# Kernel optimization log

Hardware: AMD Instinct MI355X
Metric: run time of the kernel (lower is better)

The kernel has to match this reference:

```python
import jax, jax.numpy as jnp
import numpy as np

T, B, IN, H, OUT = 16384, 1, 32, 512, 1


def setup_inputs() -> dict:
    key = jax.random.key(0)
    ks = jax.random.split(key, 7)
    s = 0.05
    return {
        "input_seq": jax.random.normal(ks[0], (T, B, IN), dtype=jnp.float32),
        "W_ih": jax.random.normal(ks[1], (4 * H, IN), dtype=jnp.float32) * s,
        "W_hh": jax.random.normal(ks[2], (4 * H, H), dtype=jnp.float32) * s,
        "b_ih": jax.random.normal(ks[3], (4 * H,), dtype=jnp.float32) * s,
        "b_hh": jax.random.normal(ks[4], (4 * H,), dtype=jnp.float32) * s,
        "W_lin": jax.random.normal(ks[5], (OUT, H), dtype=jnp.float32) * s,
        "b_lin": jax.random.normal(ks[6], (OUT,), dtype=jnp.float32) * s,
    }


def reference(input_seq, W_ih, W_hh, b_ih, b_hh, W_lin, b_lin):
    # input_seq: [T, 1, IN]; batch=1 as hardcoded by the module's hidden_cell.
    t = input_seq.shape[0]
    x = input_seq.reshape(t, -1)  # [T, IN]
    h_dim = W_hh.shape[1]
    # Precompute input contribution to gates for all timesteps (one big GEMM).
    x_gates = x @ W_ih.T + (b_ih + b_hh)  # [T, 4H]

    def step(carry, xg):
        h, c = carry
        g = xg + W_hh @ h  # [4H]; PyTorch gate order: i, f, g, o
        i = jax.nn.sigmoid(g[:h_dim])
        f = jax.nn.sigmoid(g[h_dim:2 * h_dim])
        gg = jnp.tanh(g[2 * h_dim:3 * h_dim])
        o = jax.nn.sigmoid(g[3 * h_dim:])
        c_new = f * c + i * gg
        h_new = o * jnp.tanh(c_new)
        return (h_new, c_new), h_new

    h0 = jnp.zeros((h_dim,), dtype=input_seq.dtype)
    c0 = jnp.zeros((h_dim,), dtype=input_seq.dtype)
    _, lstm_out = jax.lax.scan(step, (h0, c0), x_gates)  # [T, H]
    predictions = lstm_out @ W_lin.T + b_lin  # [T, OUT]
    return predictions[-1]  # [OUT]
```

## Files before the change

### kernel.cpp

```cpp
#include <hip/hip_runtime.h>
#include <math.h>


#define T_STEPS 16384
#define IN_DIM  32
#define H_DIM   512
#define KWG     32
#define H_SLICE 16
#define KTOT    544
#define CHUNK   136

__device__ __forceinline__ float fast_sigmoid(float v) {
  return 1.0f / (1.0f + __expf(-v));
}
__device__ __forceinline__ float fast_tanh(float v) {
  return 2.0f / (1.0f + __expf(-2.0f * v)) - 1.0f;
}

__launch_bounds__(256, 1)
__global__ void lstm_scan_kernel(
    const float* __restrict__ x,
    const float* __restrict__ Wih,
    const float* __restrict__ Whh,
    const float* __restrict__ bih,
    const float* __restrict__ bhh,
    const float* __restrict__ Wlin,
    const float* __restrict__ blin,
    float* __restrict__ out,
    unsigned long long* pub)
{
  const int wg  = blockIdx.x;
  const int tid = threadIdx.x;
  const int w   = tid >> 6;
  const int l   = tid & 63;

  __shared__ __align__(16) float hshm[KTOT];
  __shared__ float red[256];

  const int R = (l >> 4) * H_DIM + wg * H_SLICE + (l & 15);

  float wreg[CHUNK];
  #pragma unroll
  for (int j = 0; j < CHUNK; ++j) {
    const int k = w * CHUNK + j;
    wreg[j] = (k < H_DIM) ? Whh[R * H_DIM + k]
                          : Wih[R * IN_DIM + (k - H_DIM)];
  }
  const float bias = (w == 0) ? (bih[R] + bhh[R]) : 0.0f;

  float c = 0.0f;

  const int  e0 = tid * 2, e1 = tid * 2 + 1;
  const bool own0 = (e0 >> 4) == wg, own1 = (e1 >> 4) == wg;
  if (own0) hshm[e0] = 0.0f;
  if (own1) hshm[e1] = 0.0f;

  for (int t = 0; t < T_STEPS; ++t) {
    float xv = (tid < IN_DIM) ? x[t * IN_DIM + tid] : 0.0f;

    {
      const unsigned long long* p = pub + (t & 1) * H_DIM;
      const unsigned int tg = (unsigned int)t;
      bool need0 = !own0, need1 = !own1;
      while (need0 | need1) {
        if (need0) {
          unsigned long long u = __hip_atomic_load(p + e0, __ATOMIC_RELAXED,
                                                   __HIP_MEMORY_SCOPE_AGENT);
          if ((unsigned int)(u >> 32) == tg) {
            hshm[e0] = __uint_as_float((unsigned int)u);
            need0 = false;
          }
        }
        if (need1) {
          unsigned long long u = __hip_atomic_load(p + e1, __ATOMIC_RELAXED,
                                                   __HIP_MEMORY_SCOPE_AGENT);
          if ((unsigned int)(u >> 32) == tg) {
            hshm[e1] = __uint_as_float((unsigned int)u);
            need1 = false;
          }
        }
      }
      if (tid < IN_DIM) hshm[H_DIM + tid] = xv;
    }
    __syncthreads();

    const float4* hv = (const float4*)(hshm + w * CHUNK);
    float a0 = 0.f, a1 = 0.f, a2 = 0.f, a3 = 0.f;
    #pragma unroll
    for (int q = 0; q < CHUNK / 4; ++q) {
      const float4 h4 = hv[q];
      a0 = fmaf(wreg[4 * q + 0], h4.x, a0);
      a1 = fmaf(wreg[4 * q + 1], h4.y, a1);
      a2 = fmaf(wreg[4 * q + 2], h4.z, a2);
      a3 = fmaf(wreg[4 * q + 3], h4.w, a3);
    }
    red[w * 64 + l] = (a0 + a1) + (a2 + a3);
    __syncthreads();

    if (w == 0) {
      const float g = bias + red[l] + red[64 + l] + red[128 + l] + red[192 + l];
      const int j = l & 15;
      const float gi = __shfl(g, j, 64);
      const float gf = __shfl(g, j + 16, 64);
      const float gg = __shfl(g, j + 32, 64);
      const float go = __shfl(g, j + 48, 64);
      if (l < H_SLICE) {
        const float ig = fast_sigmoid(gi);
        const float fg = fast_sigmoid(gf);
        const float gt = fast_tanh(gg);
        const float og = fast_sigmoid(go);
        c = fg * c + ig * gt;
        const float h = og * fast_tanh(c);
        hshm[wg * H_SLICE + l] = h;
        const unsigned long long u =
            ((unsigned long long)(unsigned int)(t + 1) << 32) |
            (unsigned long long)__float_as_uint(h);
        __hip_atomic_store(pub + ((t + 1) & 1) * H_DIM + wg * H_SLICE + l, u,
                           __ATOMIC_RELAXED, __HIP_MEMORY_SCOPE_AGENT);
      }
    }
  }

  if (wg == 0) {
    const unsigned long long* p = pub + (T_STEPS & 1) * H_DIM;
    const unsigned int tg = (unsigned int)T_STEPS;
    bool need0 = !own0, need1 = !own1;
    while (need0 | need1) {
      if (need0) {
        unsigned long long u = __hip_atomic_load(p + e0, __ATOMIC_RELAXED,
                                                 __HIP_MEMORY_SCOPE_AGENT);
        if ((unsigned int)(u >> 32) == tg) {
          hshm[e0] = __uint_as_float((unsigned int)u);
          need0 = false;
        }
      }
      if (need1) {
        unsigned long long u = __hip_atomic_load(p + e1, __ATOMIC_RELAXED,
                                                 __HIP_MEMORY_SCOPE_AGENT);
        if ((unsigned int)(u >> 32) == tg) {
          hshm[e1] = __uint_as_float((unsigned int)u);
          need1 = false;
        }
      }
    }
    __syncthreads();
    red[tid] = hshm[e0] * Wlin[e0] + hshm[e1] * Wlin[e1];
    __syncthreads();
    if (w == 0) {
      float s = red[l] + red[64 + l] + red[128 + l] + red[192 + l];
      #pragma unroll
      for (int off = 32; off > 0; off >>= 1) s += __shfl_down(s, off, 64);
      if (l == 0) out[0] = s + blin[0];
    }
  }
}

extern "C" void kernel_launch(void* const* d_in, const int* in_sizes, int n_in,
                              void* d_out, int out_size, void* d_ws, size_t ws_size,
                              hipStream_t stream) {
  const float* x    = (const float*)d_in[0];
  const float* Wih  = (const float*)d_in[1];
  const float* Whh  = (const float*)d_in[2];
  const float* bih  = (const float*)d_in[3];
  const float* bhh  = (const float*)d_in[4];
  const float* Wlin = (const float*)d_in[5];
  const float* blin = (const float*)d_in[6];
  float* out = (float*)d_out;

  unsigned long long* pub = (unsigned long long*)d_ws;

  hipMemsetAsync(d_ws, 0, 8192, stream);
  hipLaunchKernelGGL(lstm_scan_kernel, dim3(KWG), dim3(256), 0, stream,
                     x, Wih, Whh, bih, bhh, Wlin, blin, out, pub);
}
```

Before: 31.92 ms.

## Place worker blocks on one XCD and poll h packets via L2-cached loads

Launches 256 blocks and keeps only every eighth, so the 32 active blocks likely share one XCD under round-robin dispatch and can exchange the hidden state through that XCD's L2 rather than across dies. Publication now uses inline-asm stores to both L2 and LLC scope. Polling reads two packets per 16-byte load, mostly at L2 scope with a periodic LLC-scope load. Gate activations are computed in parallel across lanes before the shuffles. This relies on unguaranteed block-to-XCD placement and on cache-coherence bits that visibility depends on, which risks stale reads or hangs if placement differs.

```diff
diff --git a/kernel.cpp b/kernel.cpp
--- a/kernel.cpp
+++ b/kernel.cpp
@@ -5,16 +5,56 @@
 #define T_STEPS 16384
 #define IN_DIM  32
 #define H_DIM   512
-#define KWG     32
+#define SLOTS   32
+#define GRID    256
 #define H_SLICE 16
 #define KTOT    544
 #define CHUNK   136
+
+typedef unsigned int uint32x4 __attribute__((ext_vector_type(4)));
 
 __device__ __forceinline__ float fast_sigmoid(float v) {
   return 1.0f / (1.0f + __expf(-v));
 }
 __device__ __forceinline__ float fast_tanh(float v) {
   return 2.0f / (1.0f + __expf(-2.0f * v)) - 1.0f;
+}
+
+__device__ __forceinline__ void store_pkt_llc(unsigned long long* p,
+                                              unsigned long long v) {
+  asm volatile("global_store_dwordx2 %0, %1, off sc0 sc1"
+               :: "v"(p), "v"(v) : "memory");
+}
+__device__ __forceinline__ void store_pkt_l2(unsigned long long* p,
+                                             unsigned long long v) {
+  asm volatile("global_store_dwordx2 %0, %1, off sc0"
+               :: "v"(p), "v"(v) : "memory");
+}
+__device__ __forceinline__ uint32x4 load_pkt2_l2(const unsigned long long* p) {
+  uint32x4 r;
+  asm volatile("global_load_dwordx4 %0, %1, off sc0\n\ts_waitcnt vmcnt(0)"
+               : "=&v"(r) : "v"(p) : "memory");
+  return r;
+}
+__device__ __forceinline__ uint32x4 load_pkt2_llc(const unsigned long long* p) {
+  uint32x4 r;
+  asm volatile("global_load_dwordx4 %0, %1, off sc0 sc1\n\ts_waitcnt vmcnt(0)"
+               : "=&v"(r) : "v"(p) : "memory");
+  return r;
+}
+
+__device__ __forceinline__ void poll_pkts(const unsigned long long* p,
+                                          unsigned int tg,
+                                          float* d0, float* d1) {
+  unsigned int spin = 0;
+  for (;;) {
+    uint32x4 r = ((++spin & 7u) != 0u) ? load_pkt2_l2(p) : load_pkt2_llc(p);
+    if (r.y == tg && r.w == tg) {
+      *d0 = __uint_as_float(r.x);
+      *d1 = __uint_as_float(r.z);
+      return;
+    }
+  }
 }
 
 __launch_bounds__(256, 1)
@@ -29,7 +69,10 @@
     float* __restrict__ out,
     unsigned long long* pub)
 {
-  const int wg  = blockIdx.x;
+  const int bx = blockIdx.x;
+  if (bx & 7) return;
+  const int slot = bx >> 3;
+
   const int tid = threadIdx.x;
   const int w   = tid >> 6;
   const int l   = tid & 63;
@@ -37,7 +80,7 @@
   __shared__ __align__(16) float hshm[KTOT];
   __shared__ float red[256];
 
-  const int R = (l >> 4) * H_DIM + wg * H_SLICE + (l & 15);
+  const int R = (l >> 4) * H_DIM + slot * H_SLICE + (l & 15);
 
   float wreg[CHUNK];
   #pragma unroll
@@ -50,38 +93,18 @@
 
   float c = 0.0f;
 
-  const int  e0 = tid * 2, e1 = tid * 2 + 1;
-  const bool own0 = (e0 >> 4) == wg, own1 = (e1 >> 4) == wg;
-  if (own0) hshm[e0] = 0.0f;
-  if (own1) hshm[e1] = 0.0f;
+  const int  e0  = tid * 2;
+  const bool own = ((tid >> 3) == slot);
+  if (own) { hshm[e0] = 0.0f; hshm[e0 + 1] = 0.0f; }
 
   for (int t = 0; t < T_STEPS; ++t) {
     float xv = (tid < IN_DIM) ? x[t * IN_DIM + tid] : 0.0f;
 
-    {
-      const unsigned long long* p = pub + (t & 1) * H_DIM;
-      const unsigned int tg = (unsigned int)t;
-      bool need0 = !own0, need1 = !own1;
-      while (need0 | need1) {
-        if (need0) {
-          unsigned long long u = __hip_atomic_load(p + e0, __ATOMIC_RELAXED,
-                                                   __HIP_MEMORY_SCOPE_AGENT);
-          if ((unsigned int)(u >> 32) == tg) {
-            hshm[e0] = __uint_as_float((unsigned int)u);
-            need0 = false;
-          }
-        }
-        if (need1) {
-          unsigned long long u = __hip_atomic_load(p + e1, __ATOMIC_RELAXED,
-                                                   __HIP_MEMORY_SCOPE_AGENT);
-          if ((unsigned int)(u >> 32) == tg) {
-            hshm[e1] = __uint_as_float((unsigned int)u);
-            need1 = false;
-          }
-        }
-      }
-      if (tid < IN_DIM) hshm[H_DIM + tid] = xv;
+    if (!own) {
+      poll_pkts(pub + (t & 1) * H_DIM + e0, (unsigned int)t,
+                &hshm[e0], &hshm[e0 + 1]);
     }
+    if (tid < IN_DIM) hshm[H_DIM + tid] = xv;
     __syncthreads();
 
     const float4* hv = (const float4*)(hshm + w * CHUNK);
@@ -99,52 +122,34 @@
 
     if (w == 0) {
       const float g = bias + red[l] + red[64 + l] + red[128 + l] + red[192 + l];
+      const float act = (l < 32 || l >= 48) ? fast_sigmoid(g) : fast_tanh(g);
       const int j = l & 15;
-      const float gi = __shfl(g, j, 64);
-      const float gf = __shfl(g, j + 16, 64);
-      const float gg = __shfl(g, j + 32, 64);
-      const float go = __shfl(g, j + 48, 64);
+      const float ig = __shfl(act, j, 64);
+      const float fg = __shfl(act, j + 16, 64);
+      const float gt = __shfl(act, j + 32, 64);
+      const float og = __shfl(act, j + 48, 64);
       if (l < H_SLICE) {
-        const float ig = fast_sigmoid(gi);
-        const float fg = fast_sigmoid(gf);
-        const float gt = fast_tanh(gg);
-        const float og = fast_sigmoid(go);
         c = fg * c + ig * gt;
         const float h = og * fast_tanh(c);
-        hshm[wg * H_SLICE + l] = h;
+        hshm[slot * H_SLICE + l] = h;
+        unsigned long long* dst =
+            pub + ((t + 1) & 1) * H_DIM + slot * H_SLICE + l;
         const unsigned long long u =
             ((unsigned long long)(unsigned int)(t + 1) << 32) |
             (unsigned long long)__float_as_uint(h);
-        __hip_atomic_store(pub + ((t + 1) & 1) * H_DIM + wg * H_SLICE + l, u,
-                           __ATOMIC_RELAXED, __HIP_MEMORY_SCOPE_AGENT);
+        store_pkt_llc(dst, u);
+        store_pkt_l2(dst, u);
       }
     }
   }
 
-  if (wg == 0) {
-    const unsigned long long* p = pub + (T_STEPS & 1) * H_DIM;
-    const unsigned int tg = (unsigned int)T_STEPS;
-    bool need0 = !own0, need1 = !own1;
-    while (need0 | need1) {
-      if (need0) {
-        unsigned long long u = __hip_atomic_load(p + e0, __ATOMIC_RELAXED,
-                                                 __HIP_MEMORY_SCOPE_AGENT);
-        if ((unsigned int)(u >> 32) == tg) {
-          hshm[e0] = __uint_as_float((unsigned int)u);
-          need0 = false;
-        }
-      }
-      if (need1) {
-        unsigned long long u = __hip_atomic_load(p + e1, __ATOMIC_RELAXED,
-                                                 __HIP_MEMORY_SCOPE_AGENT);
-        if ((unsigned int)(u >> 32) == tg) {
-          hshm[e1] = __uint_as_float((unsigned int)u);
-          need1 = false;
-        }
-      }
+  if (slot == 0) {
+    if (!own) {
+      poll_pkts(pub + (T_STEPS & 1) * H_DIM + e0, (unsigned int)T_STEPS,
+                &hshm[e0], &hshm[e0 + 1]);
     }
     __syncthreads();
-    red[tid] = hshm[e0] * Wlin[e0] + hshm[e1] * Wlin[e1];
+    red[tid] = hshm[e0] * Wlin[e0] + hshm[e0 + 1] * Wlin[e0 + 1];
     __syncthreads();
     if (w == 0) {
       float s = red[l] + red[64 + l] + red[128 + l] + red[192 + l];
@@ -170,6 +175,6 @@
   unsigned long long* pub = (unsigned long long*)d_ws;
 
   hipMemsetAsync(d_ws, 0, 8192, stream);
-  hipLaunchKernelGGL(lstm_scan_kernel, dim3(KWG), dim3(256), 0, stream,
+  hipLaunchKernelGGL(lstm_scan_kernel, dim3(GRID), dim3(256), 0, stream,
                      x, Wih, Whh, bih, bhh, Wlin, blin, out, pub);
 }
```

Measured after the change: 37.81 ms. 1.18x slower.
